# Performance work log

Hardware: AMD Instinct MI355X
Metric: run time of the kernel (lower is better)

The kernel has to match this reference:

```python
import jax, jax.numpy as jnp
import numpy as np


def setup_inputs() -> dict:
    key = jax.random.key(0)
    k1, k2 = jax.random.split(key)
    B, C, D = 8192, 8192, 256
    x = jax.random.normal(k1, (B, D), dtype=jnp.float32)
    y = jax.random.normal(k2, (C, D), dtype=jnp.float32)
    gamma = jnp.ones((), dtype=jnp.float32)
    return {"x": x, "y": y, "gamma": gamma}


def reference(x, y, gamma):
    # RBF kernel: exp(-gamma * ||x_i - y_j||^2), shape (B, C).
    # avoiding the O(B*C*D) broadcast-diff intermediate of the naive form.
    x2 = jnp.sum(x * x, axis=-1)          # (B,)
    y2 = jnp.sum(y * y, axis=-1)          # (C,)
    xy = jnp.einsum('bd,cd->bc', x, y)    # (B, C) GEMM
    sq_dist = x2[:, None] + y2[None, :] - 2.0 * xy
    sq_dist = jnp.maximum(sq_dist, 0.0)   # guard tiny negatives from cancellation
    return jnp.exp(-gamma * sq_dist)
```

## Files before the change

### kernel.cpp

```cpp
#include <hip/hip_runtime.h>
#include <hip/hip_bf16.h>

typedef __bf16 bf16_t;
typedef __attribute__((ext_vector_type(8))) __bf16 bf16x8;
typedef __attribute__((ext_vector_type(4))) __bf16 bf16x4;
typedef __attribute__((ext_vector_type(4))) float floatx4;

#define NB 8192
#define NC 8192
#define ND 256
#define BM 128
#define BN 128
#define BK 32

typedef __attribute__((address_space(3))) void lds_void_t;
typedef __attribute__((address_space(1))) void gl_void_t;

__global__ __launch_bounds__(256) void prep_kernel(
    const float* __restrict__ x, const float* __restrict__ y,
    bf16_t* __restrict__ xb, bf16_t* __restrict__ yb,
    float* __restrict__ x2, float* __restrict__ y2)
{
    int t    = threadIdx.x;
    int wave = t >> 6;
    int lane = t & 63;
    int row  = blockIdx.x * 4 + wave;

    const float* src;
    bf16_t* dst;
    float* nrm;
    int r;
    if (row < NB) { src = x; dst = xb; nrm = x2; r = row; }
    else          { src = y; dst = yb; nrm = y2; r = row - NB; }

    float4 v = ((const float4*)(src + (size_t)r * ND))[lane];
    float ss = v.x * v.x + v.y * v.y + v.z * v.z + v.w * v.w;

    bf16x4 o;
    o.x = (__bf16)v.x; o.y = (__bf16)v.y; o.z = (__bf16)v.z; o.w = (__bf16)v.w;
    ((bf16x4*)(dst + (size_t)r * ND))[lane] = o;

    #pragma unroll
    for (int off = 32; off >= 1; off >>= 1)
        ss += __shfl_xor(ss, off, 64);
    if (lane == 0) nrm[r] = ss;
}

__global__ __launch_bounds__(256) void rbf_gemm_kernel(
    const bf16_t* __restrict__ xb, const bf16_t* __restrict__ yb,
    const float* __restrict__ x2, const float* __restrict__ y2,
    const float* __restrict__ gamma_p, float* __restrict__ out)
{
    __shared__ bf16_t lA[BM * BK];
    __shared__ bf16_t lB[BN * BK];

    const int t    = threadIdx.x;
    const int lane = t & 63;
    const int wave = t >> 6;
    const int wm   = wave >> 1;
    const int wn   = wave & 1;
    const int quad = lane >> 4;
    const int l15  = lane & 15;

    const int bm = blockIdx.x * BM;
    const int bn = blockIdx.y * BN;

    const float gamma = *gamma_p;

    floatx4 acc[4][4];
    #pragma unroll
    for (int i = 0; i < 4; ++i)
        #pragma unroll
        for (int j = 0; j < 4; ++j)
            acc[i][j] = (floatx4){0.f, 0.f, 0.f, 0.f};

    const char* gA = (const char*)xb + (size_t)bm * (ND * 2);
    const char* gB = (const char*)yb + (size_t)bn * (ND * 2);

    for (int kt = 0; kt < ND / BK; ++kt) {
        __syncthreads();
        #pragma unroll
        for (int c = 0; c < 2; ++c) {
            const int li  = c * 256 + t;
            const int row = li >> 2;
            const int kb  = (li & 3) * 16;
            const size_t goff = (size_t)row * (ND * 2) + kt * (BK * 2) + kb;
            __builtin_amdgcn_global_load_lds(
                (gl_void_t*)(gA + goff),
                (lds_void_t*)((char*)lA + (size_t)li * 16), 16, 0, 0);
            __builtin_amdgcn_global_load_lds(
                (gl_void_t*)(gB + goff),
                (lds_void_t*)((char*)lB + (size_t)li * 16), 16, 0, 0);
        }
        __syncthreads();

        bf16x8 af[4], bfr[4];
        #pragma unroll
        for (int i = 0; i < 4; ++i) {
            const int ar = wm * 64 + i * 16 + l15;
            af[i]  = *(const bf16x8*)((const char*)lA + ar * (BK * 2) + quad * 16);
            const int br = wn * 64 + i * 16 + l15;
            bfr[i] = *(const bf16x8*)((const char*)lB + br * (BK * 2) + quad * 16);
        }
        #pragma unroll
        for (int i = 0; i < 4; ++i)
            #pragma unroll
            for (int j = 0; j < 4; ++j)
                acc[i][j] = __builtin_amdgcn_mfma_f32_16x16x32_bf16(
                    af[i], bfr[j], acc[i][j], 0, 0, 0);
    }

    #pragma unroll
    for (int i = 0; i < 4; ++i) {
        const int grow0 = bm + wm * 64 + i * 16 + quad * 4;
        float xn[4];
        #pragma unroll
        for (int r = 0; r < 4; ++r) xn[r] = x2[grow0 + r];
        #pragma unroll
        for (int j = 0; j < 4; ++j) {
            const int gcol = bn + wn * 64 + j * 16 + l15;
            const float yn = y2[gcol];
            #pragma unroll
            for (int r = 0; r < 4; ++r) {
                float sq = xn[r] + yn - 2.0f * acc[i][j][r];
                sq = fmaxf(sq, 0.0f);
                out[(size_t)(grow0 + r) * NC + gcol] = __expf(-gamma * sq);
            }
        }
    }
}

extern "C" void kernel_launch(void* const* d_in, const int* in_sizes, int n_in,
                              void* d_out, int out_size, void* d_ws, size_t ws_size,
                              hipStream_t stream) {
    const float* x = (const float*)d_in[0];
    const float* y = (const float*)d_in[1];
    const float* gamma = (const float*)d_in[2];
    float* out = (float*)d_out;

    bf16_t* xb = (bf16_t*)d_ws;
    bf16_t* yb = xb + (size_t)NB * ND;
    float*  x2 = (float*)(yb + (size_t)NC * ND);
    float*  y2 = x2 + NB;

    prep_kernel<<<dim3((NB + NC) / 4), dim3(256), 0, stream>>>(x, y, xb, yb, x2, y2);
    rbf_gemm_kernel<<<dim3(NB / BM, NC / BN), dim3(256), 0, stream>>>(
        xb, yb, x2, y2, gamma, out);
}
```

Baseline: 297.5 us.

## Double-buffer LDS tiles to overlap global loads with MFMA compute

Splits the A and B shared-memory tiles into two buffers. The loads for the next K-step, issued with global_load_lds, now start before the current buffer is read, and each iteration has one barrier instead of two. The aim is to hide global-to-LDS latency behind the MFMA work in this short K loop. It doubles LDS use per block, which could lower occupancy, and the compiler may still insert conservative memory waits that limit the overlap.

```diff
diff --git a/kernel.cpp b/kernel.cpp
--- a/kernel.cpp
+++ b/kernel.cpp
@@ -12,6 +12,7 @@
 #define BM 128
 #define BN 128
 #define BK 32
+#define NKT (ND / BK)
 
 typedef __attribute__((address_space(3))) void lds_void_t;
 typedef __attribute__((address_space(1))) void gl_void_t;
@@ -51,8 +52,8 @@
     const float* __restrict__ x2, const float* __restrict__ y2,
     const float* __restrict__ gamma_p, float* __restrict__ out)
 {
-    __shared__ bf16_t lA[BM * BK];
-    __shared__ bf16_t lB[BN * BK];
+    __shared__ bf16_t lA[2][BM * BK];
+    __shared__ bf16_t lB[2][BN * BK];
 
     const int t    = threadIdx.x;
     const int lane = t & 63;
@@ -77,30 +78,45 @@
     const char* gA = (const char*)xb + (size_t)bm * (ND * 2);
     const char* gB = (const char*)yb + (size_t)bn * (ND * 2);
 
-    for (int kt = 0; kt < ND / BK; ++kt) {
+    const int li0  = t;
+    const int li1  = 256 + t;
+    const int row0 = li0 >> 2, kb0 = (li0 & 3) * 16;
+    const int row1 = li1 >> 2, kb1 = (li1 & 3) * 16;
+
+    auto stage = [&](int kt, int buf) {
+        const size_t g0 = (size_t)row0 * (ND * 2) + kt * (BK * 2) + kb0;
+        const size_t g1 = (size_t)row1 * (ND * 2) + kt * (BK * 2) + kb1;
+        __builtin_amdgcn_global_load_lds(
+            (gl_void_t*)(gA + g0),
+            (lds_void_t*)((char*)&lA[buf][0] + (size_t)li0 * 16), 16, 0, 0);
+        __builtin_amdgcn_global_load_lds(
+            (gl_void_t*)(gB + g0),
+            (lds_void_t*)((char*)&lB[buf][0] + (size_t)li0 * 16), 16, 0, 0);
+        __builtin_amdgcn_global_load_lds(
+            (gl_void_t*)(gA + g1),
+            (lds_void_t*)((char*)&lA[buf][0] + (size_t)li1 * 16), 16, 0, 0);
+        __builtin_amdgcn_global_load_lds(
+            (gl_void_t*)(gB + g1),
+            (lds_void_t*)((char*)&lB[buf][0] + (size_t)li1 * 16), 16, 0, 0);
+    };
+
+    stage(0, 0);
+
+    #pragma unroll
+    for (int kt = 0; kt < NKT; ++kt) {
         __syncthreads();
-        #pragma unroll
-        for (int c = 0; c < 2; ++c) {
-            const int li  = c * 256 + t;
-            const int row = li >> 2;
-            const int kb  = (li & 3) * 16;
-            const size_t goff = (size_t)row * (ND * 2) + kt * (BK * 2) + kb;
-            __builtin_amdgcn_global_load_lds(
-                (gl_void_t*)(gA + goff),
-                (lds_void_t*)((char*)lA + (size_t)li * 16), 16, 0, 0);
-            __builtin_amdgcn_global_load_lds(
-                (gl_void_t*)(gB + goff),
-                (lds_void_t*)((char*)lB + (size_t)li * 16), 16, 0, 0);
-        }
-        __syncthreads();
+        if (kt + 1 < NKT) stage(kt + 1, (kt + 1) & 1);
+
+        const bf16_t* sA = &lA[kt & 1][0];
+        const bf16_t* sB = &lB[kt & 1][0];
 
         bf16x8 af[4], bfr[4];
         #pragma unroll
         for (int i = 0; i < 4; ++i) {
             const int ar = wm * 64 + i * 16 + l15;
-            af[i]  = *(const bf16x8*)((const char*)lA + ar * (BK * 2) + quad * 16);
+            af[i]  = *(const bf16x8*)((const char*)sA + ar * (BK * 2) + quad * 16);
             const int br = wn * 64 + i * 16 + l15;
-            bfr[i] = *(const bf16x8*)((const char*)lB + br * (BK * 2) + quad * 16);
+            bfr[i] = *(const bf16x8*)((const char*)sB + br * (BK * 2) + quad * 16);
         }
         #pragma unroll
         for (int i = 0; i < 4; ++i)
```

New measurement: 302.7 us. No clear change (+1.7%).

## Pre-swizzle bf16 operands into MFMA fragment layout and load directly to registers

Applied to the files above, without the earlier changes.

The prep kernel now writes x and y in a tiled layout where each 16-row group and k-tile forms a contiguous 1KB block, arranged so every lane's MFMA fragment is one 16-byte load. The GEMM kernel drops shared memory and barriers entirely and loads fragments straight from global memory into double-buffered registers, prefetching the next k-tile during the current MFMAs. The epilogue also vectorizes the x-norm load and uses nontemporal stores for the large output. The trade-off is that operands are no longer shared between waves through LDS, so each wave fetches its own A/B fragments, which raises global and L2 traffic and register pressure.

```diff
diff --git a/kernel.cpp b/kernel.cpp
--- a/kernel.cpp
+++ b/kernel.cpp
@@ -9,16 +9,13 @@
 #define NB 8192
 #define NC 8192
 #define ND 256
+#define NKT 8
 #define BM 128
 #define BN 128
-#define BK 32
-
-typedef __attribute__((address_space(3))) void lds_void_t;
-typedef __attribute__((address_space(1))) void gl_void_t;
 
 __global__ __launch_bounds__(256) void prep_kernel(
     const float* __restrict__ x, const float* __restrict__ y,
-    bf16_t* __restrict__ xb, bf16_t* __restrict__ yb,
+    bf16_t* __restrict__ xs, bf16_t* __restrict__ ys,
     float* __restrict__ x2, float* __restrict__ y2)
 {
     int t    = threadIdx.x;
@@ -30,15 +27,22 @@
     bf16_t* dst;
     float* nrm;
     int r;
-    if (row < NB) { src = x; dst = xb; nrm = x2; r = row; }
-    else          { src = y; dst = yb; nrm = y2; r = row - NB; }
+    if (row < NB) { src = x; dst = xs; nrm = x2; r = row; }
+    else          { src = y; dst = ys; nrm = y2; r = row - NB; }
 
     float4 v = ((const float4*)(src + (size_t)r * ND))[lane];
     float ss = v.x * v.x + v.y * v.y + v.z * v.z + v.w * v.w;
 
     bf16x4 o;
     o.x = (__bf16)v.x; o.y = (__bf16)v.y; o.z = (__bf16)v.z; o.w = (__bf16)v.w;
-    ((bf16x4*)(dst + (size_t)r * ND))[lane] = o;
+
+    const int g  = r >> 4;
+    const int rr = r & 15;
+    const int kt = lane >> 3;
+    const int q  = (lane >> 1) & 3;
+    const int h  = (lane & 1) * 8;
+    char* p = (char*)dst + (((size_t)(g * NKT + kt)) << 10) + q * 256 + rr * 16 + h;
+    *(bf16x4*)p = o;
 
     #pragma unroll
     for (int off = 32; off >= 1; off >>= 1)
@@ -47,13 +51,10 @@
 }
 
 __global__ __launch_bounds__(256) void rbf_gemm_kernel(
-    const bf16_t* __restrict__ xb, const bf16_t* __restrict__ yb,
+    const bf16_t* __restrict__ xs, const bf16_t* __restrict__ ys,
     const float* __restrict__ x2, const float* __restrict__ y2,
     const float* __restrict__ gamma_p, float* __restrict__ out)
 {
-    __shared__ bf16_t lA[BM * BK];
-    __shared__ bf16_t lB[BN * BK];
-
     const int t    = threadIdx.x;
     const int lane = t & 63;
     const int wave = t >> 6;
@@ -74,57 +75,49 @@
         for (int j = 0; j < 4; ++j)
             acc[i][j] = (floatx4){0.f, 0.f, 0.f, 0.f};
 
-    const char* gA = (const char*)xb + (size_t)bm * (ND * 2);
-    const char* gB = (const char*)yb + (size_t)bn * (ND * 2);
+    const char* aBase = (const char*)xs
+        + (((size_t)((bm >> 4) + wm * 4) * NKT) << 10) + (size_t)lane * 16;
+    const char* bBase = (const char*)ys
+        + (((size_t)((bn >> 4) + wn * 4) * NKT) << 10) + (size_t)lane * 16;
 
-    for (int kt = 0; kt < ND / BK; ++kt) {
-        __syncthreads();
-        #pragma unroll
-        for (int c = 0; c < 2; ++c) {
-            const int li  = c * 256 + t;
-            const int row = li >> 2;
-            const int kb  = (li & 3) * 16;
-            const size_t goff = (size_t)row * (ND * 2) + kt * (BK * 2) + kb;
-            __builtin_amdgcn_global_load_lds(
-                (gl_void_t*)(gA + goff),
-                (lds_void_t*)((char*)lA + (size_t)li * 16), 16, 0, 0);
-            __builtin_amdgcn_global_load_lds(
-                (gl_void_t*)(gB + goff),
-                (lds_void_t*)((char*)lB + (size_t)li * 16), 16, 0, 0);
-        }
-        __syncthreads();
-
-        bf16x8 af[4], bfr[4];
+    bf16x8 af[2][4], bfv[2][4];
+    auto ldset = [&](int kt, int buf) {
         #pragma unroll
         for (int i = 0; i < 4; ++i) {
-            const int ar = wm * 64 + i * 16 + l15;
-            af[i]  = *(const bf16x8*)((const char*)lA + ar * (BK * 2) + quad * 16);
-            const int br = wn * 64 + i * 16 + l15;
-            bfr[i] = *(const bf16x8*)((const char*)lB + br * (BK * 2) + quad * 16);
+            af[buf][i]  = *(const bf16x8*)(aBase + i * (NKT * 1024) + kt * 1024);
+            bfv[buf][i] = *(const bf16x8*)(bBase + i * (NKT * 1024) + kt * 1024);
         }
+    };
+
+    ldset(0, 0);
+    #pragma unroll
+    for (int kt = 0; kt < NKT; ++kt) {
+        const int cb = kt & 1;
+        if (kt + 1 < NKT) ldset(kt + 1, cb ^ 1);
         #pragma unroll
         for (int i = 0; i < 4; ++i)
             #pragma unroll
             for (int j = 0; j < 4; ++j)
                 acc[i][j] = __builtin_amdgcn_mfma_f32_16x16x32_bf16(
-                    af[i], bfr[j], acc[i][j], 0, 0, 0);
+                    af[cb][i], bfv[cb][j], acc[i][j], 0, 0, 0);
     }
 
     #pragma unroll
     for (int i = 0; i < 4; ++i) {
         const int grow0 = bm + wm * 64 + i * 16 + quad * 4;
-        float xn[4];
-        #pragma unroll
-        for (int r = 0; r < 4; ++r) xn[r] = x2[grow0 + r];
+        const float4 xn = *(const float4*)(x2 + grow0);
         #pragma unroll
         for (int j = 0; j < 4; ++j) {
             const int gcol = bn + wn * 64 + j * 16 + l15;
             const float yn = y2[gcol];
+            float* op = out + (size_t)grow0 * NC + gcol;
+            const float xr[4] = {xn.x, xn.y, xn.z, xn.w};
             #pragma unroll
             for (int r = 0; r < 4; ++r) {
-                float sq = xn[r] + yn - 2.0f * acc[i][j][r];
+                float sq = xr[r] + yn - 2.0f * acc[i][j][r];
                 sq = fmaxf(sq, 0.0f);
-                out[(size_t)(grow0 + r) * NC + gcol] = __expf(-gamma * sq);
+                __builtin_nontemporal_store(__expf(-gamma * sq),
+                                            op + (size_t)r * NC);
             }
         }
     }
@@ -138,12 +131,12 @@
     const float* gamma = (const float*)d_in[2];
     float* out = (float*)d_out;
 
-    bf16_t* xb = (bf16_t*)d_ws;
-    bf16_t* yb = xb + (size_t)NB * ND;
-    float*  x2 = (float*)(yb + (size_t)NC * ND);
+    bf16_t* xs = (bf16_t*)d_ws;
+    bf16_t* ys = xs + (size_t)NB * ND;
+    float*  x2 = (float*)(ys + (size_t)NC * ND);
     float*  y2 = x2 + NB;
 
-    prep_kernel<<<dim3((NB + NC) / 4), dim3(256), 0, stream>>>(x, y, xb, yb, x2, y2);
+    prep_kernel<<<dim3((NB + NC) / 4), dim3(256), 0, stream>>>(x, y, xs, ys, x2, y2);
     rbf_gemm_kernel<<<dim3(NB / BM, NC / BN), dim3(256), 0, stream>>>(
-        xb, yb, x2, y2, gamma, out);
+        xs, ys, x2, y2, gamma, out);
 }
```

Result: slower. 327.9 us (+10.2%).
